# Kernel tuning notes

Measured on AMD Instinct MI355X. Metric: run time of the kernel, lower is better.

## Reference

```python
import jax, jax.numpy as jnp
import numpy as np
from jax.scipy.linalg import cholesky, solve_triangular

SIGMA2 = 0.001   # likelihood.variance (fixed in source)
JITTER = 1e-5


def hankel(v, L):
    # Direct windowed gather; math-identical to the one-hot matmul in the source.
    Nv, Dv = v.shape
    idx = jnp.arange(Nv - L + 1)[:, None] + jnp.arange(L)[None, :]  # [Nv-L+1, L]
    return v[idx].reshape(Nv - L + 1, L * Dv)


def _sqdist(A, B):
    # ||a-b||^2, clipped for numerical safety
    d = jnp.sum(A * A, 1)[:, None] + jnp.sum(B * B, 1)[None, :] - 2.0 * A @ B.T
    return jnp.maximum(d, 0.0)


def _psi_stats(Z, Xmu, Xvar, l2, variance):
    # RBF (ARD) expected-kernel statistics (GPflow conventions).
    N = Xmu.shape[0]
    # psi0: E[k(x,x)] = variance per point, summed over N
    psi0 = jnp.asarray(N, Xmu.dtype) * variance
    # psi1[n,m] = var * prod_q (1+s/l2)^-1/2 * exp(-0.5 (mu-z)^2/(l2+s))
    denom = l2 + Xvar                                        # [N,D]
    logdet1 = -0.5 * jnp.sum(jnp.log1p(Xvar / l2), axis=1)   # [N]
    quad1 = -0.5 * jnp.sum((Xmu[:, None, :] - Z[None, :, :]) ** 2 / denom[:, None, :], axis=2)  # [N,M]
    psi1 = variance * jnp.exp(logdet1[:, None] + quad1)      # [N,M]
    # psi2[n,m,k] = var^2 * prod_q (1+2s/l2)^-1/2
    #   * exp(-(zm-zk)^2/(4 l2) - (mu - (zm+zk)/2)^2 / (2s + l2))
    a = 1.0 / (2.0 * Xvar + l2)                              # [N,D]
    cn = variance ** 2 * jnp.exp(-0.5 * jnp.sum(jnp.log1p(2.0 * Xvar / l2), axis=1))  # [N]
    Zs = Z / (2.0 * jnp.sqrt(l2))
    dZ2 = _sqdist(Zs, Zs)                                    # [M,M], (zm-zk)^2/(4 l2)
    # expand (mu - zbar)^2 * a  without a [N,M,M,D] tensor
    T1 = jnp.sum(a * Xmu * Xmu, axis=1)                      # [N]
    T2 = (a * Xmu) @ Z.T                                     # [N,M]
    T3 = a @ (Z * Z).T                                       # [N,M]
    T4 = jnp.einsum('nq,mq,kq->nmk', a, Z, Z)                # [N,M,M]
    quad2 = (T1[:, None, None] - T2[:, :, None] - T2[:, None, :]
             + 0.25 * (T3[:, :, None] + T3[:, None, :]) + 0.5 * T4)  # [N,M,M]
    psi2 = jnp.sum(cn[:, None, None] * jnp.exp(-dZ2[None, :, :] - quad2), axis=0)  # [M,M]
    return psi0, psi1, psi2


def build_likelihood(X_mean, X_var, Z, lengthscales, variance, Lt):
    N_tot, Q = X_mean.shape
    M = Z.shape[0]
    N = N_tot - Lt
    sigma2 = jnp.asarray(SIGMA2, X_mean.dtype)
    sigma = jnp.sqrt(sigma2)
    l2 = lengthscales ** 2

    X_m = hankel(X_mean[:N_tot - 1], Lt)   # [N, Lt*Q]
    X_v = hankel(X_var[:N_tot - 1], Lt)
    X_mo, X_vo = X_mean[Lt:], X_var[Lt:]   # [N, Q]
    X_mb, X_vb = X_mean[:Lt], X_var[:Lt]   # [Lt, Q]

    Kuu = variance * jnp.exp(-0.5 * _sqdist(Z / lengthscales, Z / lengthscales)) \
          + JITTER * jnp.eye(M, dtype=X_mean.dtype)
    psi0, psi1, psi2 = _psi_stats(Z, X_m, X_v, l2, variance)

    L = cholesky(Kuu, lower=True)
    A = solve_triangular(L, psi1.T, lower=True) / sigma            # [M,N]
    tmp = solve_triangular(L, psi2, lower=True)
    AAT = solve_triangular(L, tmp.T, lower=True) / sigma2          # [M,M]
    B = AAT + jnp.eye(M, dtype=X_mean.dtype)
    LB = cholesky(B, lower=True)
    log_det_B = 2.0 * jnp.sum(jnp.log(jnp.diag(LB)))
    c = solve_triangular(LB, A @ X_mo, lower=True) / sigma         # [M,Q]

    NQ = jnp.asarray(N * Q, X_mean.dtype)
    two_pi = jnp.asarray(2.0 * np.pi, X_mean.dtype)
    ent = 0.5 * jnp.sum(jnp.log(X_vo)) + 0.5 * NQ * jnp.log(two_pi)
    ent2 = -jnp.asarray(Lt * Q, X_mean.dtype) * jnp.log(two_pi) \
           - 0.5 * jnp.sum(X_mb ** 2 + X_vb)

    bound = -0.5 * NQ * jnp.log(two_pi * sigma2)
    bound += -0.5 / sigma2 * (jnp.sum(X_vo) + jnp.sum(X_mo ** 2))
    bound += -0.5 * Q * (psi0 / sigma2 - jnp.trace(AAT))
    bound += -0.5 * Q * log_det_B
    bound += 0.5 * jnp.sum(c ** 2)
    bound += ent + ent2
    return bound


def setup_inputs() -> dict:
    key = jax.random.key(0)
    k1, k2, k3 = jax.random.split(key, 3)
    N, Q, Lt, M = 4096, 4, 8, 128
    D = Lt * Q
    X_mean = jax.random.normal(k1, (N + Lt, Q), dtype=jnp.float32)
    X_var = jax.random.uniform(k2, (N + Lt, Q), dtype=jnp.float32, minval=0.1, maxval=1.0)
    Z = jax.random.normal(k3, (M, D), dtype=jnp.float32)
    lengthscales = 2.0 * jnp.ones((D,), dtype=jnp.float32)
    variance = jnp.asarray(1.0, dtype=jnp.float32)
    return {"X_mean": X_mean, "X_var": X_var, "Z": Z,
            "lengthscales": lengthscales, "variance": variance, "Lt": Lt}


def reference(X_mean, X_var, Z, lengthscales, variance, Lt):
    return build_likelihood(X_mean, X_var, Z, lengthscales, variance, Lt)
```

## Files before the change

### kernel.cpp

```cpp
#include <hip/hip_runtime.h>

#define NN   4096
#define NQ   (NN*4)
#define QQ   4
#define LTT  8
#define DD   32
#define MM   128
#define SIG2 0.001f
#define JIT  1e-5f
#define LOG2E 1.4426950408889634f

typedef _Float16 half8 __attribute__((ext_vector_type(8)));
typedef float    f32x4 __attribute__((ext_vector_type(4)));

__device__ __forceinline__ float fexp2(float x) { return exp2f(x); }

__device__ __forceinline__ float rlane(float v, int l) {
    return __uint_as_float(__builtin_amdgcn_readlane(__float_as_uint(v), l));
}

__global__ __launch_bounds__(256) void prepstatic_kernel(
    const float* __restrict__ Xm, const float* __restrict__ Xv,
    const float* __restrict__ Zg, const float* __restrict__ ls,
    const float* __restrict__ varp,
    float4* __restrict__ pk4, _Float16* __restrict__ bh,
    float* __restrict__ L1p, float* __restrict__ bbp, float* __restrict__ sumsP,
    float* __restrict__ Kuu, float* __restrict__ sp, _Float16* __restrict__ Zh,
    float* __restrict__ Yg, float* __restrict__ scalars, int* __restrict__ cnt)
{
    int b = blockIdx.x, tid = threadIdx.x;
    if (b < 16) {
        __shared__ float ra[256], rb[256], rc[256];
        int n = b*256 + tid;
        float var = varp[0];
        float slog2 = 0.f, slog1 = 0.f, T1 = 0.f, c0 = 0.f;
        #pragma unroll 8
        for (int q = 0; q < DD; ++q) {
            float xm = Xm[n*QQ + q];
            float xv = Xv[n*QQ + q];
            float l  = ls[q];
            float l2 = l*l;
            float a    = 1.0f / (2.0f*xv + l2);
            float dinv = 1.0f / (l2 + xv);
            float4 v;
            v.x = LOG2E * a * xm;
            v.y = LOG2E * (-0.25f * a);
            v.z = dinv;
            v.w = -2.0f * dinv * xm;
            pk4[n*DD + q] = v;
            bh[n*DD + q] = (_Float16)(0.5f * LOG2E * (1.0f/l2 - a));
            slog2 += log1pf(2.0f*xv/l2);
            slog1 += log1pf(xv/l2);
            T1    += a*xm*xm;
            c0    += dinv*xm*xm;
        }
        L1p[n] = 0.5f * LOG2E * (2.0f*logf(var) - 0.5f*slog2 - T1);
        bbp[n] = logf(var) - 0.5f*slog1 - 0.5f*c0;
        float s1 = 0.f, s2 = 0.f, s3 = 0.f;
        #pragma unroll
        for (int c = 0; c < QQ; ++c) {
            float mo = Xm[(n+LTT)*QQ + c];
            float vo = Xv[(n+LTT)*QQ + c];
            s1 += vo + mo*mo;
            s2 += logf(vo);
        }
        if (n < LTT) {
            #pragma unroll
            for (int c = 0; c < QQ; ++c) {
                float mb = Xm[n*QQ+c], vb = Xv[n*QQ+c];
                s3 += mb*mb + vb;
            }
        }
        ra[tid]=s1; rb[tid]=s2; rc[tid]=s3;
        __syncthreads();
        for (int s = 128; s; s >>= 1) {
            if (tid < s) { ra[tid]+=ra[tid+s]; rb[tid]+=rb[tid+s]; rc[tid]+=rc[tid+s]; }
            __syncthreads();
        }
        if (tid == 0) { sumsP[b*3+0]=ra[0]; sumsP[b*3+1]=rb[0]; sumsP[b*3+2]=rc[0]; }
    } else if (b < 80) {
        int idx = (b-16)*256 + tid;
        int i = idx >> 7, j = idx & 127;
        float var = varp[0];
        float s = 0.f;
        for (int q = 0; q < DD; ++q) {
            float l = ls[q];
            float d = (Zg[i*DD+q] - Zg[j*DD+q]) / l;
            s += d*d;
        }
        float v = var * __expf(-0.5f*s);
        if (i == j) v += JIT;
        Kuu[idx] = v;
    } else {
        if (tid < MM) {
            float s = 0.f;
            for (int q = 0; q < DD; ++q) {
                float l = ls[q]; float z = Zg[tid*DD+q];
                s += z*z / (4.0f*l*l);
            }
            sp[tid] = LOG2E * s;
        }
        for (int e = tid; e < MM*DD; e += 256) Zh[e] = (_Float16)Zg[e];
        for (int e = tid; e < 512; e += 256) Yg[e] = 0.f;
        if (tid < 8) scalars[tid] = 0.f;
        if (tid == 0) *cnt = 0;
    }
}

__global__ __launch_bounds__(256) void k1_kernel(
    const float* __restrict__ Xm, const float* __restrict__ Zg,
    const float4* __restrict__ pk4, const float* __restrict__ L1p,
    const float* __restrict__ bbp, const float* __restrict__ sp,
    float* __restrict__ r_g, float* __restrict__ Yg, float* __restrict__ psi2)
{
    __shared__ float Zl[MM*33];
    __shared__ float yredl[MM*QQ];
    int tid = threadIdx.x;
    { int e = blockIdx.x*64 + tid; if (tid < 64) psi2[e] = 0.f; }
    for (int e = tid; e < MM*DD; e += 256)
        Zl[(e>>5)*33 + (e&31)] = Zg[e];
    __syncthreads();
    int m = tid & 127, half = tid >> 7;
    float zr[DD];
    #pragma unroll
    for (int q = 0; q < DD; ++q) zr[q] = Zl[m*33 + q];
    float sm = sp[m];
    float y0=0.f, y1=0.f, y2=0.f, y3=0.f;
    int n0 = blockIdx.x*16 + half*8;
    for (int i = 0; i < 8; ++i) {
        int n = n0 + i;
        float L1n = L1p[n], bbn = bbp[n];
        const float4* pkn = pk4 + n*DD;
        float racc = 0.f, q1 = 0.f;
        #pragma unroll
        for (int q = 0; q < DD; ++q) {
            float4 v = pkn[q];
            float z = zr[q];
            racc = fmaf(v.x, z, racc);
            racc = fmaf(v.y, z*z, racc);
            float t = fmaf(v.z, z, v.w);
            q1 = fmaf(t, z, q1);
        }
        r_g[n*MM + m] = L1n + racc - sm;
        float p1 = __expf(fmaf(-0.5f, q1, bbn));
        float4 xo = *(const float4*)(Xm + (LTT+n)*QQ);
        y0 = fmaf(p1, xo.x, y0); y1 = fmaf(p1, xo.y, y1);
        y2 = fmaf(p1, xo.z, y2); y3 = fmaf(p1, xo.w, y3);
    }
    if (half == 0) {
        yredl[m*4+0]=y0; yredl[m*4+1]=y1; yredl[m*4+2]=y2; yredl[m*4+3]=y3;
    }
    __syncthreads();
    if (half == 1) {
        yredl[m*4+0]+=y0; yredl[m*4+1]+=y1; yredl[m*4+2]+=y2; yredl[m*4+3]+=y3;
    }
    __syncthreads();
    for (int e = tid; e < 512; e += 256) atomicAdd(&Yg[e], yredl[e]);
}

template<int NT>
__device__ __forceinline__ void dev_chol(float* mat, int tid)
{
    int wv = tid >> 6, ln = tid & 63;
    for (int p = 0; p < 8; ++p) {
        int base = p*16;
        if (wv == 0) {
            int r0 = base + ln, r1 = r0 + 64;
            bool h0 = r0 < 128, h1 = r1 < 128;
            float a0[16], a1[16];
            #pragma unroll
            for (int c = 0; c < 16; ++c) {
                a0[c] = h0 ? mat[r0*132 + base + c] : 0.f;
                a1[c] = h1 ? mat[r1*132 + base + c] : 0.f;
            }
            #pragma unroll
            for (int kk = 0; kk < 16; ++kk) {
                float d   = rlane(a0[kk], kk);
                float rdk = rsqrtf(d);
                float sq  = d * rdk;
                a0[kk] = (ln == kk) ? sq : a0[kk] * rdk;
                a1[kk] *= rdk;
                #pragma unroll
                for (int j = kk+1; j < 16; ++j) {
                    float ljv = rlane(a0[kk], j);
                    a0[j] = fmaf(-a0[kk], ljv, a0[j]);
                    a1[j] = fmaf(-a1[kk], ljv, a1[j]);
                }
            }
            #pragma unroll
            for (int c = 0; c < 16; ++c) {
                if (h0) mat[r0*132 + base + c] = a0[c];
                if (h1) mat[r1*132 + base + c] = a1[c];
            }
        }
        __syncthreads();
        int S = 112 - base;
        if (S > 0) {
            int T = S >> 2, nb = base + 16;
            int nT = (T*(T+1)) >> 1;
            for (int t = tid; t < nT; t += NT) {
                int ti = (int)(0.5f*(sqrtf(8.f*(float)t + 1.f) - 1.f));
                if ((ti+1)*(ti+2)/2 <= t) ++ti;
                else if (ti*(ti+1)/2 > t) --ti;
                int tj = t - ((ti*(ti+1))>>1);
                int i0 = nb + ti*4, j0 = nb + tj*4;
                float ac[4][4];
                #pragma unroll
                for (int r = 0; r < 4; ++r)
                    #pragma unroll
                    for (int s = 0; s < 4; ++s) ac[r][s] = mat[(i0+r)*132 + j0 + s];
                #pragma unroll
                for (int c4 = 0; c4 < 4; ++c4) {
                    float4 av[4], bv[4];
                    #pragma unroll
                    for (int r = 0; r < 4; ++r) {
                        av[r] = *(const float4*)&mat[(i0+r)*132 + base + c4*4];
                        bv[r] = *(const float4*)&mat[(j0+r)*132 + base + c4*4];
                    }
                    #pragma unroll
                    for (int r = 0; r < 4; ++r)
                        #pragma unroll
                        for (int s = 0; s < 4; ++s)
                            ac[r][s] -= av[r].x*bv[s].x + av[r].y*bv[s].y
                                      + av[r].z*bv[s].z + av[r].w*bv[s].w;
                }
                #pragma unroll
                for (int r = 0; r < 4; ++r)
                    #pragma unroll
                    for (int s = 0; s < 4; ++s) mat[(i0+r)*132 + j0 + s] = ac[r][s];
            }
        }
        __syncthreads();
    }
}

template<int NT>
__device__ __forceinline__ void dev_dinv(const float* mat, float* dinvb, int tid)
{
    int wv = tid >> 6, ln = tid & 63;
    if (ln < 16) {
        int c = ln;
        for (int bd = wv; bd < 8; bd += NT/64) {
            int base = bd*16;
            float x[16];
            #pragma unroll
            for (int i = 0; i < 16; ++i) {
                float dii = mat[(base+i)*132 + base + i];
                float s = 0.f;
                #pragma unroll
                for (int j = 0; j < i; ++j) s += mat[(base+i)*132 + base + j] * x[j];
                float v;
                if (i < c) v = 0.f;
                else if (i == c) v = 1.0f / dii;
                else v = -s / dii;
                x[i] = v;
            }
            #pragma unroll
            for (int i = 0; i < 16; ++i) dinvb[bd*256 + i*16 + c] = x[i];
        }
    }
    __syncthreads();
}

template<int C>
__device__ __forceinline__ void dev_bsolve(const float* mat, const float* dinvb,
                                           float* tmp, float* rhs, int tid)
{
    const int AT = 16*C;
    int r = tid / C, cc = tid % C;
    for (int bi = 7; bi >= 0; --bi) {
        float acc = 0.f;
        if (tid < AT) {
            acc = rhs[(bi*16+r)*C + cc];
            for (int bj = bi+1; bj < 8; ++bj) {
                #pragma unroll
                for (int kk = 0; kk < 16; ++kk)
                    acc -= mat[(bj*16+kk)*132 + bi*16 + r] * rhs[(bj*16+kk)*C + cc];
            }
        }
        __syncthreads();
        if (tid < AT) tmp[r*C + cc] = acc;
        __syncthreads();
        if (tid < AT) {
            float w = 0.f;
            #pragma unroll
            for (int kk = 0; kk < 16; ++kk)
                w += dinvb[bi*256 + kk*16 + r] * tmp[kk*C + cc];
            rhs[(bi*16+r)*C + cc] = w;
        }
        __syncthreads();
    }
}

__global__ __launch_bounds__(512) void psi2chol_kernel(
    const _Float16* __restrict__ Zh, const float* __restrict__ r_g,
    const _Float16* __restrict__ bh, float* __restrict__ psi2,
    const float* __restrict__ Kuu, float* __restrict__ Lg,
    float* __restrict__ Dinvg, float* __restrict__ scalars)
{
    __shared__ float shm[19456];
    int tid = threadIdx.x;
    if (blockIdx.x == 0) {
        float* mat   = shm;
        float* dinvb = shm + 16896;
        float* red   = shm + 18944;
        for (int e = tid; e < 16384; e += 512) mat[(e>>7)*132 + (e&127)] = Kuu[e];
        __syncthreads();
        dev_chol<512>(mat, tid);
        red[tid] = (tid < 128) ? logf(mat[tid*132 + tid]) : 0.f;
        __syncthreads();
        for (int s = 256; s; s >>= 1) { if (tid < s) red[tid] += red[tid+s]; __syncthreads(); }
        if (tid == 0) scalars[0] = red[0];
        dev_dinv<512>(mat, dinvb, tid);
        for (int e = tid; e < 16384; e += 512) Lg[e] = mat[(e>>7)*132 + (e&127)];
        for (int e = tid; e < 2048; e += 512) Dinvg[e] = dinvb[e];
    } else {
        float (*pacc)[64][4] = (float(*)[64][4])shm;
        int w = tid >> 6, l = tid & 63, lm = l & 15, lg = l >> 4;
        int b = blockIdx.x - 1;
        int t = b % 36, nq = b / 36;
        int kt = (int)(0.5f*(sqrtf(8.f*(float)t + 1.f) - 1.f));
        if ((kt+1)*(kt+2)/2 <= t) ++kt;
        else if (kt*(kt+1)/2 > t) --kt;
        int mt = t - ((kt*(kt+1))>>1);

        half8 Bf = ((const half8*)Zh)[(kt*16 + lm)*4 + lg];
        half8 Zm = ((const half8*)Zh)[(mt*16 + lm)*4 + lg];
        f32x4 z4; z4[0]=0.f; z4[1]=0.f; z4[2]=0.f; z4[3]=0.f;
        f32x4 acc0 = z4, acc1 = z4;
        int n0g = nq*128 + w*16;
        const float* rbase = r_g + (size_t)n0g*MM;
        const half8* bbase = (const half8*)bh + (size_t)n0g*4;
        for (int i = 0; i < 16; i += 2) {
            half8 bf0 = bbase[i*4 + lg];
            half8 bf1 = bbase[i*4 + 4 + lg];
            const float* rn0 = rbase + i*MM;
            f32x4 rm0 = *(const f32x4*)(rn0 + mt*16 + lg*4);
            f32x4 rm1 = *(const f32x4*)(rn0 + MM + mt*16 + lg*4);
            float rk0 = rn0[kt*16 + lm];
            float rk1 = rn0[MM + kt*16 + lm];
            half8 A0 = Zm * bf0;
            half8 A1 = Zm * bf1;
            f32x4 p0 = __builtin_amdgcn_mfma_f32_16x16x32_f16(A0, Bf, z4, 0, 0, 0);
            f32x4 p1 = __builtin_amdgcn_mfma_f32_16x16x32_f16(A1, Bf, z4, 0, 0, 0);
            acc0[0] += fexp2(p0[0] + rm0[0] + rk0);
            acc0[1] += fexp2(p0[1] + rm0[1] + rk0);
            acc0[2] += fexp2(p0[2] + rm0[2] + rk0);
            acc0[3] += fexp2(p0[3] + rm0[3] + rk0);
            acc1[0] += fexp2(p1[0] + rm1[0] + rk1);
            acc1[1] += fexp2(p1[1] + rm1[1] + rk1);
            acc1[2] += fexp2(p1[2] + rm1[2] + rk1);
            acc1[3] += fexp2(p1[3] + rm1[3] + rk1);
        }
        #pragma unroll
        for (int j = 0; j < 4; ++j) pacc[w][l][j] = acc0[j] + acc1[j];
        __syncthreads();
        if (tid < 256) {
            int ll = tid >> 2, j = tid & 3;
            float s = 0.f;
            #pragma unroll
            for (int ww = 0; ww < 8; ++ww) s += pacc[ww][ll][j];
            int row = mt*16 + (ll >> 4)*4 + j;
            int col = kt*16 + (ll & 15);
            atomicAdd(&psi2[row*MM + col], s);
            if (mt != kt) atomicAdd(&psi2[col*MM + row], s);
        }
    }
}

__global__ __launch_bounds__(512) void cholG_kernel(
    const float* __restrict__ Kuu, const float* __restrict__ psi2,
    const float* __restrict__ Yg, const float* __restrict__ Lg,
    const float* __restrict__ Dinvg, const float* __restrict__ varp,
    const float* __restrict__ sumsP,
    float* __restrict__ scalars, int* __restrict__ cnt, float* __restrict__ out)
{
    __shared__ float mat[128*132];
    __shared__ float dinvb[8*256];
    __shared__ float rhs[128*8];
    __shared__ float tmp[128];
    __shared__ float red[512];
    int tid = threadIdx.x;
    if (blockIdx.x == 0) {
        for (int e = tid; e < 16384; e += 512)
            mat[(e>>7)*132 + (e&127)] = Kuu[e] + (1.0f/SIG2)*psi2[e];
        __syncthreads();
        dev_chol<512>(mat, tid);
        red[tid] = (tid < 128) ? logf(mat[tid*132 + tid]) : 0.f;
        __syncthreads();
        for (int s = 256; s; s >>= 1) { if (tid < s) red[tid] += red[tid+s]; __syncthreads(); }
        if (tid == 0) scalars[1] = red[0];
        dev_dinv<512>(mat, dinvb, tid);
        rhs[tid & 511] = Yg[tid & 511];
        __syncthreads();
        if (tid < 64) {
            int r = tid >> 2, cc = tid & 3;
            for (int bi = 0; bi < 8; ++bi) {
                float a0 = rhs[(bi*16+r)*4 + cc], a1 = 0.f, a2 = 0.f, a3 = 0.f;
                for (int bk = 0; bk < bi; ++bk) {
                    const float* mrow = &mat[(bi*16+r)*132 + bk*16];
                    const float* rb   = &rhs[bk*64 + cc];
                    #pragma unroll
                    for (int kk = 0; kk < 16; kk += 4) {
                        a0 = fmaf(-mrow[kk+0], rb[(kk+0)*4], a0);
                        a1 = fmaf(-mrow[kk+1], rb[(kk+1)*4], a1);
                        a2 = fmaf(-mrow[kk+2], rb[(kk+2)*4], a2);
                        a3 = fmaf(-mrow[kk+3], rb[(kk+3)*4], a3);
                    }
                }
                float acc = (a0+a1)+(a2+a3);
                float w = 0.f;
                #pragma unroll
                for (int kk = 0; kk < 16; ++kk)
                    w += dinvb[bi*256 + r*16 + kk] * __shfl(acc, kk*4 + cc, 64);
                rhs[(bi*16+r)*4 + cc] = w;
            }
        }
        __syncthreads();
        { float v = rhs[tid & 511]; red[tid] = v*v; }
        __syncthreads();
        for (int s = 256; s; s >>= 1) { if (tid < s) red[tid] += red[tid+s]; __syncthreads(); }
        if (tid == 0) scalars[2] = red[0];
    } else {
        int c0 = (blockIdx.x - 1) * 8;
        for (int e = tid; e < 16384; e += 512) mat[(e>>7)*132 + (e&127)] = Lg[e];
        for (int e = tid; e < 2048; e += 512) dinvb[e] = Dinvg[e];
        for (int e = tid; e < 1024; e += 512) {
            int i = e >> 3, cc = e & 7;
            rhs[e] = (i == c0 + cc) ? 1.0f : 0.0f;
        }
        __syncthreads();
        dev_bsolve<8>(mat, dinvb, tmp, rhs, tid);
        int i = tid & 127, cp = (tid >> 7) & 1, jh = tid >> 8;
        float vv0=0.f, vv1=0.f, vv2=0.f, vv3=0.f;
        for (int j = jh*64; j < jh*64 + 64; ++j) {
            float pj = psi2[j*MM + i];
            vv0 = fmaf(pj, rhs[j*8 + cp*4 + 0], vv0);
            vv1 = fmaf(pj, rhs[j*8 + cp*4 + 1], vv1);
            vv2 = fmaf(pj, rhs[j*8 + cp*4 + 2], vv2);
            vv3 = fmaf(pj, rhs[j*8 + cp*4 + 3], vv3);
        }
        float part = rhs[i*8 + cp*4 + 0]*vv0 + rhs[i*8 + cp*4 + 1]*vv1
                   + rhs[i*8 + cp*4 + 2]*vv2 + rhs[i*8 + cp*4 + 3]*vv3;
        red[tid] = part;
        __syncthreads();
        for (int s = 256; s; s >>= 1) { if (tid < s) red[tid] += red[tid+s]; __syncthreads(); }
        if (tid == 0) atomicAdd(&scalars[3], red[0]);
    }
    if (tid == 0) {
        __threadfence();
        int old = atomicAdd(cnt, 1);
        if (old == 16) {
            float ldK  = scalars[0];
            float ldG  = atomicAdd(&scalars[1], 0.0f);
            float c2s  = atomicAdd(&scalars[2], 0.0f);
            float trr  = atomicAdd(&scalars[3], 0.0f);
            float s1=0.f, s2=0.f, s3=0.f;
            for (int b2 = 0; b2 < 16; ++b2) {
                s1 += sumsP[b2*3+0]; s2 += sumsP[b2*3+1]; s3 += sumsP[b2*3+2];
            }
            float var = varp[0];
            float trAAT   = trr / SIG2;
            float logdetB = 2.0f * (ldG - ldK);
            float sumc2   = c2s / (SIG2*SIG2);
            float psi0    = (float)NN * var;
            const float LOG2PI = 1.837877066409345f;
            float NQf = (float)NQ;
            float bound = -0.5f*NQf*(LOG2PI + logf(SIG2));
            bound += -0.5f/SIG2 * s1;
            bound += -0.5f*(float)QQ*(psi0/SIG2 - trAAT);
            bound += -0.5f*(float)QQ*logdetB;
            bound += 0.5f*sumc2;
            bound += 0.5f*s2 + 0.5f*NQf*LOG2PI;
            bound += -(float)(LTT*QQ)*LOG2PI - 0.5f*s3;
            out[0] = bound;
        }
    }
}

extern "C" void kernel_launch(void* const* d_in, const int* in_sizes, int n_in,
                              void* d_out, int out_size, void* d_ws, size_t ws_size,
                              hipStream_t stream)
{
    (void)in_sizes; (void)n_in; (void)out_size; (void)ws_size;
    const float* Xm   = (const float*)d_in[0];
    const float* Xv   = (const float*)d_in[1];
    const float* Zg   = (const float*)d_in[2];
    const float* ls   = (const float*)d_in[3];
    const float* varp = (const float*)d_in[4];

    float* p = (float*)d_ws;
    float4*   pk4   = (float4*)p;       p += NN*DD*4;
    float*    r_g   = p;                p += NN*MM;
    _Float16* bh    = (_Float16*)p;     p += NN*DD/2;
    _Float16* Zh    = (_Float16*)p;     p += MM*DD/2;
    float*    L1p   = p;                p += NN;
    float*    bbp   = p;                p += NN;
    float*    sp    = p;                p += MM;
    float*    Kuu   = p;                p += MM*MM;
    float*    Lg    = p;                p += MM*MM;
    float*    Dinvg = p;                p += 2048;
    float*    psi2  = p;                p += MM*MM;
    float*    Yg    = p;                p += 512;
    float*    sumsP = p;                p += 64;
    float*    scalars = p;              p += 8;
    int*      cnt   = (int*)p;          p += 4;

    prepstatic_kernel<<<81, 256, 0, stream>>>(Xm, Xv, Zg, ls, varp,
                                              pk4, bh, L1p, bbp, sumsP, Kuu, sp, Zh,
                                              Yg, scalars, cnt);
    k1_kernel<<<256, 256, 0, stream>>>(Xm, Zg, pk4, L1p, bbp, sp, r_g, Yg, psi2);
    psi2chol_kernel<<<1153, 512, 0, stream>>>(Zh, r_g, bh, psi2, Kuu, Lg, Dinvg, scalars);
    cholG_kernel<<<17, 512, 0, stream>>>(Kuu, psi2, Yg, Lg, Dinvg, varp, sumsP,
                                         scalars, cnt, (float*)d_out);
}
```

Baseline: 177.5 us.

## Fuse prep into k1, compute full Kuu inverse once, simplify trace pass

Merges the per-point precompute kernel into k1, so the packed coefficients stay in shared memory and never round-trip through global memory. The psi2chol block now forms the full inverse of L (Kuu) in place, which lets the trace term be computed directly as a quadratic form with 8 blocks instead of 16 blocks each doing a blocked back-solve. Zero-initialisation moves to a single hipMemsetAsync and the partial sums go to atomics. One kernel launch and some global traffic are saved, at the cost of extra serial work in the single Cholesky block (block inversion) and an added memset node.

```diff
diff --git a/kernel.cpp b/kernel.cpp
--- a/kernel.cpp
+++ b/kernel.cpp
@@ -19,67 +19,126 @@
     return __uint_as_float(__builtin_amdgcn_readlane(__float_as_uint(v), l));
 }
 
-__global__ __launch_bounds__(256) void prepstatic_kernel(
+__global__ __launch_bounds__(256) void k1_kernel(
     const float* __restrict__ Xm, const float* __restrict__ Xv,
     const float* __restrict__ Zg, const float* __restrict__ ls,
     const float* __restrict__ varp,
-    float4* __restrict__ pk4, _Float16* __restrict__ bh,
-    float* __restrict__ L1p, float* __restrict__ bbp, float* __restrict__ sumsP,
-    float* __restrict__ Kuu, float* __restrict__ sp, _Float16* __restrict__ Zh,
-    float* __restrict__ Yg, float* __restrict__ scalars, int* __restrict__ cnt)
+    _Float16* __restrict__ bh, float* __restrict__ r_g, float* __restrict__ Yg,
+    _Float16* __restrict__ Zh, float* __restrict__ Kuu, float* __restrict__ scalars)
 {
     int b = blockIdx.x, tid = threadIdx.x;
-    if (b < 16) {
-        __shared__ float ra[256], rb[256], rc[256];
-        int n = b*256 + tid;
-        float var = varp[0];
+    if (b < 256) {
+        __shared__ float Zl[MM*33];
+        __shared__ float pkl[16][DD][4];
+        __shared__ float L1l[16], bbl[16];
+        __shared__ float lsq[DD];
+        __shared__ float yredl[MM*QQ];
+        __shared__ float redl[48];
+        for (int e = tid; e < MM*DD; e += 256)
+            Zl[(e>>5)*33 + (e&31)] = Zg[e];
+        if (tid < DD) { float l = ls[tid]; lsq[tid] = 1.0f/(l*l); }
+        __syncthreads();
+        int n0 = b*16;
+        float var  = varp[0];
+        float logv = logf(var);
+        int nl = tid >> 4;
+        int n  = n0 + nl;
         float slog2 = 0.f, slog1 = 0.f, T1 = 0.f, c0 = 0.f;
-        #pragma unroll 8
-        for (int q = 0; q < DD; ++q) {
-            float xm = Xm[n*QQ + q];
-            float xv = Xv[n*QQ + q];
-            float l  = ls[q];
-            float l2 = l*l;
+        #pragma unroll
+        for (int t2 = 0; t2 < 2; ++t2) {
+            int q = (tid & 15)*2 + t2;
+            float xm  = Xm[n*QQ + q];
+            float xv  = Xv[n*QQ + q];
+            float il2 = lsq[q];
+            float l2  = 1.0f / il2;
             float a    = 1.0f / (2.0f*xv + l2);
             float dinv = 1.0f / (l2 + xv);
-            float4 v;
-            v.x = LOG2E * a * xm;
-            v.y = LOG2E * (-0.25f * a);
-            v.z = dinv;
-            v.w = -2.0f * dinv * xm;
-            pk4[n*DD + q] = v;
-            bh[n*DD + q] = (_Float16)(0.5f * LOG2E * (1.0f/l2 - a));
-            slog2 += log1pf(2.0f*xv/l2);
-            slog1 += log1pf(xv/l2);
+            pkl[nl][q][0] = LOG2E * a * xm;
+            pkl[nl][q][1] = LOG2E * (-0.25f * a);
+            pkl[nl][q][2] = dinv;
+            pkl[nl][q][3] = -2.0f * dinv * xm;
+            bh[n*DD + q] = (_Float16)(0.5f * LOG2E * (il2 - a));
+            slog2 += log1pf(2.0f*xv*il2);
+            slog1 += log1pf(xv*il2);
             T1    += a*xm*xm;
             c0    += dinv*xm*xm;
         }
-        L1p[n] = 0.5f * LOG2E * (2.0f*logf(var) - 0.5f*slog2 - T1);
-        bbp[n] = logf(var) - 0.5f*slog1 - 0.5f*c0;
         float s1 = 0.f, s2 = 0.f, s3 = 0.f;
-        #pragma unroll
-        for (int c = 0; c < QQ; ++c) {
+        if ((tid & 15) < 4) {
+            int c = tid & 3;
             float mo = Xm[(n+LTT)*QQ + c];
             float vo = Xv[(n+LTT)*QQ + c];
-            s1 += vo + mo*mo;
-            s2 += logf(vo);
-        }
-        if (n < LTT) {
-            #pragma unroll
-            for (int c = 0; c < QQ; ++c) {
-                float mb = Xm[n*QQ+c], vb = Xv[n*QQ+c];
-                s3 += mb*mb + vb;
-            }
-        }
-        ra[tid]=s1; rb[tid]=s2; rc[tid]=s3;
-        __syncthreads();
-        for (int s = 128; s; s >>= 1) {
-            if (tid < s) { ra[tid]+=ra[tid+s]; rb[tid]+=rb[tid+s]; rc[tid]+=rc[tid+s]; }
-            __syncthreads();
-        }
-        if (tid == 0) { sumsP[b*3+0]=ra[0]; sumsP[b*3+1]=rb[0]; sumsP[b*3+2]=rc[0]; }
-    } else if (b < 80) {
-        int idx = (b-16)*256 + tid;
+            s1 = vo + mo*mo;
+            s2 = logf(vo);
+            if (n < LTT) {
+                float mb = Xm[n*QQ + c], vb = Xv[n*QQ + c];
+                s3 = mb*mb + vb;
+            }
+        }
+        #pragma unroll
+        for (int off = 1; off < 16; off <<= 1) {
+            slog2 += __shfl_xor(slog2, off, 64);
+            slog1 += __shfl_xor(slog1, off, 64);
+            T1    += __shfl_xor(T1, off, 64);
+            c0    += __shfl_xor(c0, off, 64);
+            s1    += __shfl_xor(s1, off, 64);
+            s2    += __shfl_xor(s2, off, 64);
+            s3    += __shfl_xor(s3, off, 64);
+        }
+        if ((tid & 15) == 0) {
+            L1l[nl] = 0.5f * LOG2E * (2.0f*logv - 0.5f*slog2 - T1);
+            bbl[nl] = logv - 0.5f*slog1 - 0.5f*c0;
+            redl[nl] = s1; redl[16+nl] = s2; redl[32+nl] = s3;
+        }
+        __syncthreads();
+        if (tid == 0) {
+            float a1=0.f, a2=0.f, a3=0.f;
+            for (int i2 = 0; i2 < 16; ++i2) { a1+=redl[i2]; a2+=redl[16+i2]; a3+=redl[32+i2]; }
+            atomicAdd(&scalars[4], a1);
+            atomicAdd(&scalars[5], a2);
+            atomicAdd(&scalars[6], a3);
+        }
+        int m = tid & 127, half = tid >> 7;
+        float zr[DD];
+        #pragma unroll
+        for (int q = 0; q < DD; ++q) zr[q] = Zl[m*33 + q];
+        float sm = 0.f;
+        #pragma unroll
+        for (int q = 0; q < DD; ++q) sm = fmaf(zr[q]*zr[q], lsq[q], sm);
+        sm *= 0.25f * LOG2E;
+        float y0=0.f, y1=0.f, y2=0.f, y3=0.f;
+        int nb = half*8;
+        for (int i = 0; i < 8; ++i) {
+            int nli = nb + i;
+            float L1n = L1l[nli], bbn = bbl[nli];
+            float racc = 0.f, q1 = 0.f;
+            #pragma unroll
+            for (int q = 0; q < DD; ++q) {
+                float4 v = *(const float4*)&pkl[nli][q][0];
+                float z = zr[q];
+                racc = fmaf(v.x, z, racc);
+                racc = fmaf(v.y, z*z, racc);
+                float t = fmaf(v.z, z, v.w);
+                q1 = fmaf(t, z, q1);
+            }
+            int gn = n0 + nli;
+            r_g[gn*MM + m] = L1n + racc - sm;
+            float p1 = __expf(fmaf(-0.5f, q1, bbn));
+            float4 xo = *(const float4*)(Xm + (LTT+gn)*QQ);
+            y0 = fmaf(p1, xo.x, y0); y1 = fmaf(p1, xo.y, y1);
+            y2 = fmaf(p1, xo.z, y2); y3 = fmaf(p1, xo.w, y3);
+        }
+        if (half == 0) {
+            yredl[m*4+0]=y0; yredl[m*4+1]=y1; yredl[m*4+2]=y2; yredl[m*4+3]=y3;
+        }
+        __syncthreads();
+        if (half == 1) {
+            yredl[m*4+0]+=y0; yredl[m*4+1]+=y1; yredl[m*4+2]+=y2; yredl[m*4+3]+=y3;
+        }
+        __syncthreads();
+        for (int e = tid; e < 512; e += 256) atomicAdd(&Yg[e], yredl[e]);
+    } else if (b < 320) {
+        int idx = (b-256)*256 + tid;
         int i = idx >> 7, j = idx & 127;
         float var = varp[0];
         float s = 0.f;
@@ -92,73 +151,10 @@
         if (i == j) v += JIT;
         Kuu[idx] = v;
     } else {
-        if (tid < MM) {
-            float s = 0.f;
-            for (int q = 0; q < DD; ++q) {
-                float l = ls[q]; float z = Zg[tid*DD+q];
-                s += z*z / (4.0f*l*l);
-            }
-            sp[tid] = LOG2E * s;
-        }
         for (int e = tid; e < MM*DD; e += 256) Zh[e] = (_Float16)Zg[e];
-        for (int e = tid; e < 512; e += 256) Yg[e] = 0.f;
-        if (tid < 8) scalars[tid] = 0.f;
-        if (tid == 0) *cnt = 0;
     }
 }
 
-__global__ __launch_bounds__(256) void k1_kernel(
-    const float* __restrict__ Xm, const float* __restrict__ Zg,
-    const float4* __restrict__ pk4, const float* __restrict__ L1p,
-    const float* __restrict__ bbp, const float* __restrict__ sp,
-    float* __restrict__ r_g, float* __restrict__ Yg, float* __restrict__ psi2)
-{
-    __shared__ float Zl[MM*33];
-    __shared__ float yredl[MM*QQ];
-    int tid = threadIdx.x;
-    { int e = blockIdx.x*64 + tid; if (tid < 64) psi2[e] = 0.f; }
-    for (int e = tid; e < MM*DD; e += 256)
-        Zl[(e>>5)*33 + (e&31)] = Zg[e];
-    __syncthreads();
-    int m = tid & 127, half = tid >> 7;
-    float zr[DD];
-    #pragma unroll
-    for (int q = 0; q < DD; ++q) zr[q] = Zl[m*33 + q];
-    float sm = sp[m];
-    float y0=0.f, y1=0.f, y2=0.f, y3=0.f;
-    int n0 = blockIdx.x*16 + half*8;
-    for (int i = 0; i < 8; ++i) {
-        int n = n0 + i;
-        float L1n = L1p[n], bbn = bbp[n];
-        const float4* pkn = pk4 + n*DD;
-        float racc = 0.f, q1 = 0.f;
-        #pragma unroll
-        for (int q = 0; q < DD; ++q) {
-            float4 v = pkn[q];
-            float z = zr[q];
-            racc = fmaf(v.x, z, racc);
-            racc = fmaf(v.y, z*z, racc);
-            float t = fmaf(v.z, z, v.w);
-            q1 = fmaf(t, z, q1);
-        }
-        r_g[n*MM + m] = L1n + racc - sm;
-        float p1 = __expf(fmaf(-0.5f, q1, bbn));
-        float4 xo = *(const float4*)(Xm + (LTT+n)*QQ);
-        y0 = fmaf(p1, xo.x, y0); y1 = fmaf(p1, xo.y, y1);
-        y2 = fmaf(p1, xo.z, y2); y3 = fmaf(p1, xo.w, y3);
-    }
-    if (half == 0) {
-        yredl[m*4+0]=y0; yredl[m*4+1]=y1; yredl[m*4+2]=y2; yredl[m*4+3]=y3;
-    }
-    __syncthreads();
-    if (half == 1) {
-        yredl[m*4+0]+=y0; yredl[m*4+1]+=y1; yredl[m*4+2]+=y2; yredl[m*4+3]+=y3;
-    }
-    __syncthreads();
-    for (int e = tid; e < 512; e += 256) atomicAdd(&Yg[e], yredl[e]);
-}
-
-template<int NT>
 __device__ __forceinline__ void dev_chol(float* mat, int tid)
 {
     int wv = tid >> 6, ln = tid & 63;
@@ -198,7 +194,7 @@
         if (S > 0) {
             int T = S >> 2, nb = base + 16;
             int nT = (T*(T+1)) >> 1;
-            for (int t = tid; t < nT; t += NT) {
+            for (int t = tid; t < nT; t += 512) {
                 int ti = (int)(0.5f*(sqrtf(8.f*(float)t + 1.f) - 1.f));
                 if ((ti+1)*(ti+2)/2 <= t) ++ti;
                 else if (ti*(ti+1)/2 > t) --ti;
@@ -234,86 +230,100 @@
     }
 }
 
-template<int NT>
 __device__ __forceinline__ void dev_dinv(const float* mat, float* dinvb, int tid)
 {
     int wv = tid >> 6, ln = tid & 63;
     if (ln < 16) {
-        int c = ln;
-        for (int bd = wv; bd < 8; bd += NT/64) {
-            int base = bd*16;
-            float x[16];
-            #pragma unroll
-            for (int i = 0; i < 16; ++i) {
-                float dii = mat[(base+i)*132 + base + i];
-                float s = 0.f;
-                #pragma unroll
-                for (int j = 0; j < i; ++j) s += mat[(base+i)*132 + base + j] * x[j];
-                float v;
-                if (i < c) v = 0.f;
-                else if (i == c) v = 1.0f / dii;
-                else v = -s / dii;
-                x[i] = v;
-            }
-            #pragma unroll
-            for (int i = 0; i < 16; ++i) dinvb[bd*256 + i*16 + c] = x[i];
-        }
+        int c = ln, bd = wv;
+        int base = bd*16;
+        float x[16];
+        #pragma unroll
+        for (int i = 0; i < 16; ++i) {
+            float dii = mat[(base+i)*132 + base + i];
+            float s = 0.f;
+            #pragma unroll
+            for (int j = 0; j < i; ++j) s += mat[(base+i)*132 + base + j] * x[j];
+            float v;
+            if (i < c) v = 0.f;
+            else if (i == c) v = 1.0f / dii;
+            else v = -s / dii;
+            x[i] = v;
+        }
+        #pragma unroll
+        for (int i = 0; i < 16; ++i) dinvb[bd*256 + i*16 + c] = x[i];
     }
     __syncthreads();
-}
-
-template<int C>
-__device__ __forceinline__ void dev_bsolve(const float* mat, const float* dinvb,
-                                           float* tmp, float* rhs, int tid)
-{
-    const int AT = 16*C;
-    int r = tid / C, cc = tid % C;
-    for (int bi = 7; bi >= 0; --bi) {
-        float acc = 0.f;
-        if (tid < AT) {
-            acc = rhs[(bi*16+r)*C + cc];
-            for (int bj = bi+1; bj < 8; ++bj) {
-                #pragma unroll
-                for (int kk = 0; kk < 16; ++kk)
-                    acc -= mat[(bj*16+kk)*132 + bi*16 + r] * rhs[(bj*16+kk)*C + cc];
-            }
-        }
-        __syncthreads();
-        if (tid < AT) tmp[r*C + cc] = acc;
-        __syncthreads();
-        if (tid < AT) {
-            float w = 0.f;
-            #pragma unroll
-            for (int kk = 0; kk < 16; ++kk)
-                w += dinvb[bi*256 + kk*16 + r] * tmp[kk*C + cc];
-            rhs[(bi*16+r)*C + cc] = w;
-        }
-        __syncthreads();
-    }
 }
 
 __global__ __launch_bounds__(512) void psi2chol_kernel(
     const _Float16* __restrict__ Zh, const float* __restrict__ r_g,
     const _Float16* __restrict__ bh, float* __restrict__ psi2,
     const float* __restrict__ Kuu, float* __restrict__ Lg,
-    float* __restrict__ Dinvg, float* __restrict__ scalars)
+    float* __restrict__ scalars)
 {
-    __shared__ float shm[19456];
+    __shared__ float shm[19968];
     int tid = threadIdx.x;
     if (blockIdx.x == 0) {
         float* mat   = shm;
         float* dinvb = shm + 16896;
         float* red   = shm + 18944;
+        float* tmpM  = shm + 19456;
         for (int e = tid; e < 16384; e += 512) mat[(e>>7)*132 + (e&127)] = Kuu[e];
         __syncthreads();
-        dev_chol<512>(mat, tid);
+        dev_chol(mat, tid);
         red[tid] = (tid < 128) ? logf(mat[tid*132 + tid]) : 0.f;
         __syncthreads();
         for (int s = 256; s; s >>= 1) { if (tid < s) red[tid] += red[tid+s]; __syncthreads(); }
         if (tid == 0) scalars[0] = red[0];
-        dev_dinv<512>(mat, dinvb, tid);
+        dev_dinv(mat, dinvb, tid);
+        #pragma unroll
+        for (int bi = 1; bi < 8; ++bi) {
+            const int total = bi*256;
+            const int np = (total + 511)/512;
+            float wbuf[4];
+            #pragma unroll
+            for (int ps = 0; ps < np; ++ps) {
+                int e = ps*512 + tid;
+                float Mv = 0.f;
+                int bj = e >> 8, r = (e >> 4) & 15, c = e & 15;
+                if (e < total) {
+                    #pragma unroll
+                    for (int kk = 0; kk < 16; ++kk)
+                        Mv = fmaf(mat[(bi*16+r)*132 + bj*16+kk], dinvb[bj*256 + kk*16 + c], Mv);
+                    for (int k = bj+1; k < bi; ++k)
+                        #pragma unroll
+                        for (int kk = 0; kk < 16; ++kk)
+                            Mv = fmaf(mat[(bi*16+r)*132 + k*16+kk], mat[(k*16+kk)*132 + bj*16+c], Mv);
+                }
+                __syncthreads();
+                if (e < total) tmpM[tid] = Mv;
+                __syncthreads();
+                float w = 0.f;
+                if (e < total) {
+                    int lbj = tid >> 8;
+                    #pragma unroll
+                    for (int kk = 0; kk < 16; ++kk)
+                        w = fmaf(dinvb[bi*256 + r*16 + kk], tmpM[lbj*256 + kk*16 + c], w);
+                }
+                wbuf[ps] = w;
+            }
+            __syncthreads();
+            #pragma unroll
+            for (int ps = 0; ps < np; ++ps) {
+                int e = ps*512 + tid;
+                if (e < total) {
+                    int bj = e >> 8, r = (e >> 4) & 15, c = e & 15;
+                    mat[(bi*16+r)*132 + bj*16 + c] = -wbuf[ps];
+                }
+            }
+            __syncthreads();
+        }
+        for (int e = tid; e < 2048; e += 512) {
+            int bd = e >> 8, r = (e >> 4) & 15, c = e & 15;
+            mat[(bd*16+r)*132 + bd*16 + c] = dinvb[e];
+        }
+        __syncthreads();
         for (int e = tid; e < 16384; e += 512) Lg[e] = mat[(e>>7)*132 + (e&127)];
-        for (int e = tid; e < 2048; e += 512) Dinvg[e] = dinvb[e];
     } else {
         float (*pacc)[64][4] = (float(*)[64][4])shm;
         int w = tid >> 6, l = tid & 63, lm = l & 15, lg = l >> 4;
@@ -371,27 +381,26 @@
 __global__ __launch_bounds__(512) void cholG_kernel(
     const float* __restrict__ Kuu, const float* __restrict__ psi2,
     const float* __restrict__ Yg, const float* __restrict__ Lg,
-    const float* __restrict__ Dinvg, const float* __restrict__ varp,
-    const float* __restrict__ sumsP,
+    const float* __restrict__ varp,
     float* __restrict__ scalars, int* __restrict__ cnt, float* __restrict__ out)
 {
-    __shared__ float mat[128*132];
-    __shared__ float dinvb[8*256];
-    __shared__ float rhs[128*8];
-    __shared__ float tmp[128];
-    __shared__ float red[512];
+    __shared__ float shm[20480];
     int tid = threadIdx.x;
     if (blockIdx.x == 0) {
+        float* mat   = shm;
+        float* dinvb = shm + 16896;
+        float* rhs   = shm + 18944;
+        float* red   = shm + 19456;
         for (int e = tid; e < 16384; e += 512)
             mat[(e>>7)*132 + (e&127)] = Kuu[e] + (1.0f/SIG2)*psi2[e];
         __syncthreads();
-        dev_chol<512>(mat, tid);
+        dev_chol(mat, tid);
         red[tid] = (tid < 128) ? logf(mat[tid*132 + tid]) : 0.f;
         __syncthreads();
         for (int s = 256; s; s >>= 1) { if (tid < s) red[tid] += red[tid+s]; __syncthreads(); }
         if (tid == 0) scalars[1] = red[0];
-        dev_dinv<512>(mat, dinvb, tid);
-        rhs[tid & 511] = Yg[tid & 511];
+        dev_dinv(mat, dinvb, tid);
+        rhs[tid] = Yg[tid];
         __syncthreads();
         if (tid < 64) {
             int r = tid >> 2, cc = tid & 3;
@@ -417,48 +426,54 @@
             }
         }
         __syncthreads();
-        { float v = rhs[tid & 511]; red[tid] = v*v; }
+        { float v = rhs[tid]; red[tid] = v*v; }
         __syncthreads();
         for (int s = 256; s; s >>= 1) { if (tid < s) red[tid] += red[tid+s]; __syncthreads(); }
         if (tid == 0) scalars[2] = red[0];
     } else {
-        int c0 = (blockIdx.x - 1) * 8;
-        for (int e = tid; e < 16384; e += 512) mat[(e>>7)*132 + (e&127)] = Lg[e];
-        for (int e = tid; e < 2048; e += 512) dinvb[e] = Dinvg[e];
-        for (int e = tid; e < 1024; e += 512) {
-            int i = e >> 3, cc = e & 7;
-            rhs[e] = (i == c0 + cc) ? 1.0f : 0.0f;
-        }
-        __syncthreads();
-        dev_bsolve<8>(mat, dinvb, tmp, rhs, tid);
-        int i = tid & 127, cp = (tid >> 7) & 1, jh = tid >> 8;
-        float vv0=0.f, vv1=0.f, vv2=0.f, vv3=0.f;
-        for (int j = jh*64; j < jh*64 + 64; ++j) {
-            float pj = psi2[j*MM + i];
-            vv0 = fmaf(pj, rhs[j*8 + cp*4 + 0], vv0);
-            vv1 = fmaf(pj, rhs[j*8 + cp*4 + 1], vv1);
-            vv2 = fmaf(pj, rhs[j*8 + cp*4 + 2], vv2);
-            vv3 = fmaf(pj, rhs[j*8 + cp*4 + 3], vv3);
-        }
-        float part = rhs[i*8 + cp*4 + 0]*vv0 + rhs[i*8 + cp*4 + 1]*vv1
-                   + rhs[i*8 + cp*4 + 2]*vv2 + rhs[i*8 + cp*4 + 3]*vv3;
-        red[tid] = part;
-        __syncthreads();
-        for (int s = 256; s; s >>= 1) { if (tid < s) red[tid] += red[tid+s]; __syncthreads(); }
-        if (tid == 0) atomicAdd(&scalars[3], red[0]);
+        float* psl  = shm;
+        float* lrow = shm + 16512;
+        float* redl = shm + 17552;
+        for (int e = tid; e < 16384; e += 512)
+            psl[(e>>7)*129 + (e&127)] = psi2[e];
+        __syncthreads();
+        int w = tid >> 6, l = tid & 63;
+        float kacc = 0.f;
+        for (int kk2 = 0; kk2 < 2; ++kk2) {
+            int k = (blockIdx.x - 1)*16 + w*2 + kk2;
+            lrow[w*130 + l]      = (l      <= k) ? Lg[k*MM + l]      : 0.f;
+            lrow[w*130 + l + 64] = (l + 64 <= k) ? Lg[k*MM + l + 64] : 0.f;
+            __syncthreads();
+            float wa = 0.f, wb = 0.f;
+            for (int j = 0; j <= k; ++j) {
+                float lj = lrow[w*130 + j];
+                wa = fmaf(psl[j*129 + l],      lj, wa);
+                wb = fmaf(psl[j*129 + l + 64], lj, wb);
+            }
+            float part = wa * lrow[w*130 + l] + wb * lrow[w*130 + l + 64];
+            for (int off = 32; off; off >>= 1) part += __shfl_xor(part, off, 64);
+            kacc += part;
+            __syncthreads();
+        }
+        if (l == 0) redl[w] = kacc;
+        __syncthreads();
+        if (tid == 0) {
+            float s = 0.f;
+            for (int ww = 0; ww < 8; ++ww) s += redl[ww];
+            atomicAdd(&scalars[3], s);
+        }
     }
     if (tid == 0) {
         __threadfence();
         int old = atomicAdd(cnt, 1);
-        if (old == 16) {
+        if (old == 8) {
             float ldK  = scalars[0];
             float ldG  = atomicAdd(&scalars[1], 0.0f);
             float c2s  = atomicAdd(&scalars[2], 0.0f);
             float trr  = atomicAdd(&scalars[3], 0.0f);
-            float s1=0.f, s2=0.f, s3=0.f;
-            for (int b2 = 0; b2 < 16; ++b2) {
-                s1 += sumsP[b2*3+0]; s2 += sumsP[b2*3+1]; s3 += sumsP[b2*3+2];
-            }
+            float s1   = atomicAdd(&scalars[4], 0.0f);
+            float s2   = atomicAdd(&scalars[5], 0.0f);
+            float s3   = atomicAdd(&scalars[6], 0.0f);
             float var = varp[0];
             float trAAT   = trr / SIG2;
             float logdetB = 2.0f * (ldG - ldK);
@@ -490,27 +505,18 @@
     const float* varp = (const float*)d_in[4];
 
     float* p = (float*)d_ws;
-    float4*   pk4   = (float4*)p;       p += NN*DD*4;
     float*    r_g   = p;                p += NN*MM;
     _Float16* bh    = (_Float16*)p;     p += NN*DD/2;
     _Float16* Zh    = (_Float16*)p;     p += MM*DD/2;
-    float*    L1p   = p;                p += NN;
-    float*    bbp   = p;                p += NN;
-    float*    sp    = p;                p += MM;
     float*    Kuu   = p;                p += MM*MM;
     float*    Lg    = p;                p += MM*MM;
-    float*    Dinvg = p;                p += 2048;
     float*    psi2  = p;                p += MM*MM;
     float*    Yg    = p;                p += 512;
-    float*    sumsP = p;                p += 64;
     float*    scalars = p;              p += 8;
     int*      cnt   = (int*)p;          p += 4;
 
-    prepstatic_kernel<<<81, 256, 0, stream>>>(Xm, Xv, Zg, ls, varp,
-                                              pk4, bh, L1p, bbp, sumsP, Kuu, sp, Zh,
-                                              Yg, scalars, cnt);
-    k1_kernel<<<256, 256, 0, stream>>>(Xm, Zg, pk4, L1p, bbp, sp, r_g, Yg, psi2);
-    psi2chol_kernel<<<1153, 512, 0, stream>>>(Zh, r_g, bh, psi2, Kuu, Lg, Dinvg, scalars);
-    cholG_kernel<<<17, 512, 0, stream>>>(Kuu, psi2, Yg, Lg, Dinvg, varp, sumsP,
-                                         scalars, cnt, (float*)d_out);
-}
+    hipMemsetAsync(psi2, 0, (MM*MM + 512 + 8 + 4)*sizeof(float), stream);
+    k1_kernel<<<321, 256, 0, stream>>>(Xm, Xv, Zg, ls, varp, bh, r_g, Yg, Zh, Kuu, scalars);
+    psi2chol_kernel<<<1153, 512, 0, stream>>>(Zh, r_g, bh, psi2, Kuu, Lg, scalars);
+    cholG_kernel<<<9, 512, 0, stream>>>(Kuu, psi2, Yg, Lg, varp, scalars, cnt, (float*)d_out);
+}
```

Measured after the change: 165.2 us. -7.0%, faster.
